# Optimization experiments

Hardware: AMD Instinct MI355X
Metric: run time of the kernel (lower is better)

The kernel has to match this reference:

```python
import jax, jax.numpy as jnp
import numpy as np

IN_FEATURES = 4096
OUT_FEATURES = 4096  # % 16 == 0, so pad_out = 0
BATCH, SEQ = 4, 2048


def setup_inputs() -> dict:
    key = jax.random.key(0)
    k_x, k_w, k_b = jax.random.split(key, 3)
    # int8 activations and weights (W8A8)
    x = jax.random.randint(k_x, (BATCH, SEQ, IN_FEATURES), -128, 128, dtype=jnp.int32).astype(jnp.int8)
    # weight stored as (in_features, out_features), matching qlinear.weight layout
    weight = jax.random.randint(k_w, (IN_FEATURES, OUT_FEATURES), -128, 128, dtype=jnp.int32).astype(jnp.int8)
    # a: scalar input scale; b: per-output-channel dequant/requant scale
    a = jnp.full((1, 1), 0.0123, dtype=jnp.float32)
    b = jax.random.uniform(k_b, (1, OUT_FEATURES), dtype=jnp.float32, minval=0.001, maxval=0.02)
    return {"x": x, "weight": weight, "a": a, "b": b}


def reference(x, weight, a, b):
    # x: [B, S, K] int8; weight: [K, N] int8; a: [1,1] f32; b: [1,N] f32
    x_shape = x.shape
    x2d = x.reshape(-1, x_shape[-1])
    acc = jnp.matmul(x2d, weight, preferred_element_type=jnp.int32)
    # fused dequant (scalar a) + per-channel requant (b), round-to-nearest, saturate to int8
    y_f = acc.astype(jnp.float32) * a * b  # [T, N]
    y = jnp.clip(jnp.round(y_f), -128.0, 127.0).astype(jnp.int8)
    return y.reshape(*x_shape[:-1], -1)
```

## Files before the change

### kernel.cpp

```cpp
#include <hip/hip_runtime.h>
#include <stdint.h>

#define M_DIM 8192
#define N_DIM 4096
#define K_DIM 4096
#define BM 128
#define BN 128
#define BK 64

typedef int v4i __attribute__((ext_vector_type(4)));
typedef unsigned u32;

__device__ __forceinline__ void gll16(const void* g, void* l) {
  __builtin_amdgcn_global_load_lds(
      (const __attribute__((address_space(1))) void*)g,
      (__attribute__((address_space(3))) void*)l, 16, 0, 0);
}

__device__ __forceinline__ u32 pack4(const int4 v) {
  return (v.x & 0xffu) | ((v.y & 0xffu) << 8) | ((v.z & 0xffu) << 16) |
         ((u32)(v.w & 0xffu) << 24);
}

__global__ __launch_bounds__(256) void detect_i32(const int* __restrict__ X,
                                                  u32* __restrict__ flag) {
  __shared__ int ok;
  if (threadIdx.x == 0) ok = 1;
  __syncthreads();
  int good = 1;
  for (int i = threadIdx.x; i < 1024; i += 256) {
    const int w = X[i];
    good &= (w == (int)(int8_t)(w & 0xff));
  }
  if (!good) atomicAnd(&ok, 0);
  __syncthreads();
  if (threadIdx.x == 0) *flag = (u32)ok;
}

__global__ __launch_bounds__(256) void pack_x_ad(const void* __restrict__ Xin,
                                                 u32* __restrict__ out,
                                                 const u32* __restrict__ flag) {
  const bool i32 = (*flag != 0);
  const int base = blockIdx.x * 1024 + threadIdx.x;
  if (i32) {
    const int4* in = (const int4*)Xin;
#pragma unroll
    for (int j = 0; j < 4; ++j) {
      const int idx = base + j * 256;
      out[idx] = pack4(in[idx]);
    }
  } else {
    const u32* in = (const u32*)Xin;
#pragma unroll
    for (int j = 0; j < 4; ++j) {
      const int idx = base + j * 256;
      out[idx] = in[idx];
    }
  }
}

__global__ __launch_bounds__(256) void packT_w_ad(const void* __restrict__ Wv,
                                                  int8_t* __restrict__ WT,
                                                  const u32* __restrict__ flag) {
  __shared__ u32 lds[64 * 21];
  const bool i32 = (*flag != 0);
  const int tid = threadIdx.x;
  const int tk = blockIdx.x & 63;
  const int tn = blockIdx.x >> 6;
  const int k0 = tk * 64, n0 = tn * 64;

#pragma unroll
  for (int j = 0; j < 4; ++j) {
    const int id = j * 256 + tid;
    const int k = id >> 4, c = id & 15;
    u32 word;
    if (i32) {
      const int4 v =
          *(const int4*)((const int*)Wv + (size_t)(k0 + k) * N_DIM + n0 + c * 4);
      word = pack4(v);
    } else {
      word = *(const u32*)((const int8_t*)Wv + (size_t)(k0 + k) * N_DIM + n0 +
                           c * 4);
    }
    lds[k * 21 + c] = word;
  }
  __syncthreads();
  const int kd = tid & 15, nq = tid >> 4;
  const u32 d0 = lds[(kd * 4 + 0) * 21 + nq];
  const u32 d1 = lds[(kd * 4 + 1) * 21 + nq];
  const u32 d2 = lds[(kd * 4 + 2) * 21 + nq];
  const u32 d3 = lds[(kd * 4 + 3) * 21 + nq];
  u32* outp = (u32*)WT;
#pragma unroll
  for (int i = 0; i < 4; ++i) {
    const u32 e = ((d0 >> (8 * i)) & 0xffu) | (((d1 >> (8 * i)) & 0xffu) << 8) |
                  (((d2 >> (8 * i)) & 0xffu) << 16) |
                  (((d3 >> (8 * i)) & 0xffu) << 24);
    const int n = n0 + nq * 4 + i;
    outp[(size_t)n * (K_DIM / 4) + (k0 / 4) + kd] = e;
  }
}

__device__ __forceinline__ void epilogue(const v4i acc[4][4], float a,
                                         const float* __restrict__ bScale,
                                         int* __restrict__ Y, int bm, int bn,
                                         int wm, int wn, int quad, int l16) {
  const int nBase = bn * BN + wn * 64 + l16;
  float bs[4];
#pragma unroll
  for (int ni = 0; ni < 4; ++ni) bs[ni] = bScale[nBase + ni * 16];
#pragma unroll
  for (int mi = 0; mi < 4; ++mi) {
    const int m0 = bm * BM + wm * 64 + mi * 16 + quad * 4;
#pragma unroll
    for (int r = 0; r < 4; ++r) {
      int* row = Y + (size_t)(m0 + r) * N_DIM + nBase;
#pragma unroll
      for (int ni = 0; ni < 4; ++ni) {
        float v = ((float)acc[mi][ni][r] * a) * bs[ni];
        v = rintf(v);
        v = fminf(fmaxf(v, -128.f), 127.f);
        row[ni * 16] = (int)v;
      }
    }
  }
}

__global__ __launch_bounds__(256) void gemm_packed(
    const int8_t* __restrict__ X, const int8_t* __restrict__ WT,
    const float* __restrict__ aScale, const float* __restrict__ bScale,
    int* __restrict__ Y) {
  __shared__ __align__(16) int8_t As[BM * BK];
  __shared__ __align__(16) int8_t Bs[BN * BK];
  const int tid = threadIdx.x;
  const int lane = tid & 63, wave = tid >> 6;
  const int quad = lane >> 4, l16 = lane & 15;
  const int wm = wave & 1, wn = wave >> 1;
  const int bn = blockIdx.x & 31;
  const int bm = blockIdx.x >> 5;

  const int r0 = tid >> 2;
  const int c0 = (tid & 3) * 16;
  const int8_t* Ag0 = X + (size_t)(bm * BM + r0) * K_DIM + c0;
  const int8_t* Ag1 = Ag0 + (size_t)64 * K_DIM;
  const int8_t* Bg0 = WT + (size_t)(bn * BN + r0) * K_DIM + c0;
  const int8_t* Bg1 = Bg0 + (size_t)64 * K_DIM;
  int8_t* Al0 = As + tid * 16;
  int8_t* Al1 = Al0 + 4096;
  int8_t* Bl0 = Bs + tid * 16;
  int8_t* Bl1 = Bl0 + 4096;

  v4i acc[4][4] = {};
  const int8_t* aLds = As + (wm * 64 + l16) * BK + quad * 16;
  const int8_t* bLds = Bs + (wn * 64 + l16) * BK + quad * 16;

  for (int k0 = 0; k0 < K_DIM; k0 += BK) {
    gll16(Ag0 + k0, Al0);
    gll16(Ag1 + k0, Al1);
    gll16(Bg0 + k0, Bl0);
    gll16(Bg1 + k0, Bl1);
    __syncthreads();
    v4i af[4], bf[4];
#pragma unroll
    for (int i = 0; i < 4; ++i) af[i] = *(const v4i*)(aLds + i * 16 * BK);
#pragma unroll
    for (int i = 0; i < 4; ++i) bf[i] = *(const v4i*)(bLds + i * 16 * BK);
#pragma unroll
    for (int mi = 0; mi < 4; ++mi)
#pragma unroll
      for (int ni = 0; ni < 4; ++ni)
        acc[mi][ni] = __builtin_amdgcn_mfma_i32_16x16x64_i8(
            af[mi], bf[ni], acc[mi][ni], 0, 0, 0);
    __syncthreads();
  }
  epilogue(acc, aScale[0], bScale, Y, bm, bn, wm, wn, quad, l16);
}

__global__ __launch_bounds__(256) void gemm_inA(
    const void* __restrict__ Xv, const int8_t* __restrict__ WT,
    const float* __restrict__ aScale, const float* __restrict__ bScale,
    int* __restrict__ Y, const u32* __restrict__ flag) {
  __shared__ __align__(16) int8_t As[BM * BK];
  __shared__ __align__(16) int8_t Bs[BN * BK];
  const bool i32 = (*flag != 0);
  const int tid = threadIdx.x;
  const int lane = tid & 63, wave = tid >> 6;
  const int quad = lane >> 4, l16 = lane & 15;
  const int wm = wave & 1, wn = wave >> 1;
  const int bn = blockIdx.x & 31;
  const int bm = blockIdx.x >> 5;

  const int r0 = tid >> 2;
  const int c0 = (tid & 3) * 16;
  const int8_t* Bg0 = WT + (size_t)(bn * BN + r0) * K_DIM + c0;
  const int8_t* Bg1 = Bg0 + (size_t)64 * K_DIM;
  int8_t* Al0 = As + tid * 16;
  int8_t* Al1 = Al0 + 4096;
  int8_t* Bl0 = Bs + tid * 16;
  int8_t* Bl1 = Bl0 + 4096;

  v4i acc[4][4] = {};
  const int8_t* aLds = As + (wm * 64 + l16) * BK + quad * 16;
  const int8_t* bLds = Bs + (wn * 64 + l16) * BK + quad * 16;

  if (i32) {
    const int* Xg0 = (const int*)Xv + (size_t)(bm * BM + r0) * K_DIM + c0;
    const int* Xg1 = Xg0 + (size_t)64 * K_DIM;
    for (int k0 = 0; k0 < K_DIM; k0 += BK) {
      gll16(Bg0 + k0, Bl0);
      gll16(Bg1 + k0, Bl1);
      const int4* p0 = (const int4*)(Xg0 + k0);
      const int4* p1 = (const int4*)(Xg1 + k0);
      uint4 w0, w1;
      w0.x = pack4(p0[0]); w0.y = pack4(p0[1]);
      w0.z = pack4(p0[2]); w0.w = pack4(p0[3]);
      w1.x = pack4(p1[0]); w1.y = pack4(p1[1]);
      w1.z = pack4(p1[2]); w1.w = pack4(p1[3]);
      *(uint4*)Al0 = w0;
      *(uint4*)Al1 = w1;
      __syncthreads();
      v4i af[4], bf[4];
#pragma unroll
      for (int i = 0; i < 4; ++i) af[i] = *(const v4i*)(aLds + i * 16 * BK);
#pragma unroll
      for (int i = 0; i < 4; ++i) bf[i] = *(const v4i*)(bLds + i * 16 * BK);
#pragma unroll
      for (int mi = 0; mi < 4; ++mi)
#pragma unroll
        for (int ni = 0; ni < 4; ++ni)
          acc[mi][ni] = __builtin_amdgcn_mfma_i32_16x16x64_i8(
              af[mi], bf[ni], acc[mi][ni], 0, 0, 0);
      __syncthreads();
    }
  } else {
    const int8_t* Ag0 = (const int8_t*)Xv + (size_t)(bm * BM + r0) * K_DIM + c0;
    const int8_t* Ag1 = Ag0 + (size_t)64 * K_DIM;
    for (int k0 = 0; k0 < K_DIM; k0 += BK) {
      gll16(Ag0 + k0, Al0);
      gll16(Ag1 + k0, Al1);
      gll16(Bg0 + k0, Bl0);
      gll16(Bg1 + k0, Bl1);
      __syncthreads();
      v4i af[4], bf[4];
#pragma unroll
      for (int i = 0; i < 4; ++i) af[i] = *(const v4i*)(aLds + i * 16 * BK);
#pragma unroll
      for (int i = 0; i < 4; ++i) bf[i] = *(const v4i*)(bLds + i * 16 * BK);
#pragma unroll
      for (int mi = 0; mi < 4; ++mi)
#pragma unroll
        for (int ni = 0; ni < 4; ++ni)
          acc[mi][ni] = __builtin_amdgcn_mfma_i32_16x16x64_i8(
              af[mi], bf[ni], acc[mi][ni], 0, 0, 0);
      __syncthreads();
    }
  }
  epilogue(acc, aScale[0], bScale, Y, bm, bn, wm, wn, quad, l16);
}

extern "C" void kernel_launch(void* const* d_in, const int* in_sizes, int n_in,
                              void* d_out, int out_size, void* d_ws,
                              size_t ws_size, hipStream_t stream) {
  const void* Xv = d_in[0];
  const void* Wv = d_in[1];
  const float* a = (const float*)d_in[2];
  const float* b = (const float*)d_in[3];
  int* Y = (int*)d_out;

  const size_t xB = (size_t)M_DIM * K_DIM;
  const size_t wB = (size_t)N_DIM * K_DIM;
  const int grid = (M_DIM / BM) * (N_DIM / BN);

  if (ws_size >= xB + wB + 64) {
    int8_t* Xp = (int8_t*)d_ws;
    int8_t* WT = (int8_t*)d_ws + xB;
    u32* flag = (u32*)((int8_t*)d_ws + xB + wB);
    detect_i32<<<1, 256, 0, stream>>>((const int*)Xv, flag);
    pack_x_ad<<<(M_DIM * K_DIM / 4) / 1024, 256, 0, stream>>>(Xv, (u32*)Xp,
                                                              flag);
    packT_w_ad<<<(K_DIM / 64) * (N_DIM / 64), 256, 0, stream>>>(Wv, WT, flag);
    gemm_packed<<<grid, 256, 0, stream>>>(Xp, WT, a, b, Y);
  } else if (ws_size >= wB + 64) {
    int8_t* WT = (int8_t*)d_ws;
    u32* flag = (u32*)((int8_t*)d_ws + wB);
    detect_i32<<<1, 256, 0, stream>>>((const int*)Xv, flag);
    packT_w_ad<<<(K_DIM / 64) * (N_DIM / 64), 256, 0, stream>>>(Wv, WT, flag);
    gemm_inA<<<grid, 256, 0, stream>>>(Xv, WT, a, b, Y, flag);
  } else {
    int8_t* WT = (int8_t*)d_ws;
    u32* flag = (u32*)((int8_t*)d_ws + (ws_size >= wB + 4 ? wB : 0));
    detect_i32<<<1, 256, 0, stream>>>((const int*)Xv, flag);
    packT_w_ad<<<(K_DIM / 64) * (N_DIM / 64), 256, 0, stream>>>(Wv, WT, flag);
    gemm_inA<<<grid, 256, 0, stream>>>(Xv, WT, a, b, Y, flag);
  }
}
```

Measured before the change: 431.2 us.

## Fuse X/W prepack into one kernel, drop dtype detection, swizzle LDS layout

Removes the runtime int32-vs-int8 detection kernel and its workspace-size fallbacks, and assumes inputs always arrive as int32. The X pack and the W transpose-pack are merged into a single launch, cutting two launches. The GEMM LDS staging now uses an XOR-swizzled 128-byte row layout (two logical rows per LDS row) so MFMA fragment reads avoid bank conflicts. The risks are that int8-typed inputs or a small workspace are no longer handled.

Result: no change. 431.5 us (+0.1%).

```diff
diff --git a/kernel.cpp b/kernel.cpp
--- a/kernel.cpp
+++ b/kernel.cpp
@@ -22,67 +22,31 @@
          ((u32)(v.w & 0xffu) << 24);
 }
 
-__global__ __launch_bounds__(256) void detect_i32(const int* __restrict__ X,
-                                                  u32* __restrict__ flag) {
-  __shared__ int ok;
-  if (threadIdx.x == 0) ok = 1;
-  __syncthreads();
-  int good = 1;
-  for (int i = threadIdx.x; i < 1024; i += 256) {
-    const int w = X[i];
-    good &= (w == (int)(int8_t)(w & 0xff));
-  }
-  if (!good) atomicAnd(&ok, 0);
-  __syncthreads();
-  if (threadIdx.x == 0) *flag = (u32)ok;
-}
-
-__global__ __launch_bounds__(256) void pack_x_ad(const void* __restrict__ Xin,
-                                                 u32* __restrict__ out,
-                                                 const u32* __restrict__ flag) {
-  const bool i32 = (*flag != 0);
-  const int base = blockIdx.x * 1024 + threadIdx.x;
-  if (i32) {
-    const int4* in = (const int4*)Xin;
+__global__ __launch_bounds__(256) void prepack(const int4* __restrict__ Xi,
+                                               u32* __restrict__ Xp,
+                                               const int* __restrict__ Wi,
+                                               int8_t* __restrict__ WT) {
+  __shared__ u32 lds[64 * 21];
+  const int tid = threadIdx.x;
+  if (blockIdx.x < 8192) {
+    const int base = blockIdx.x * 1024 + tid;
 #pragma unroll
     for (int j = 0; j < 4; ++j) {
       const int idx = base + j * 256;
-      out[idx] = pack4(in[idx]);
+      Xp[idx] = pack4(Xi[idx]);
     }
-  } else {
-    const u32* in = (const u32*)Xin;
-#pragma unroll
-    for (int j = 0; j < 4; ++j) {
-      const int idx = base + j * 256;
-      out[idx] = in[idx];
-    }
+    return;
   }
-}
-
-__global__ __launch_bounds__(256) void packT_w_ad(const void* __restrict__ Wv,
-                                                  int8_t* __restrict__ WT,
-                                                  const u32* __restrict__ flag) {
-  __shared__ u32 lds[64 * 21];
-  const bool i32 = (*flag != 0);
-  const int tid = threadIdx.x;
-  const int tk = blockIdx.x & 63;
-  const int tn = blockIdx.x >> 6;
+  const int bid = blockIdx.x - 8192;
+  const int tk = bid & 63;
+  const int tn = bid >> 6;
   const int k0 = tk * 64, n0 = tn * 64;
-
 #pragma unroll
   for (int j = 0; j < 4; ++j) {
     const int id = j * 256 + tid;
     const int k = id >> 4, c = id & 15;
-    u32 word;
-    if (i32) {
-      const int4 v =
-          *(const int4*)((const int*)Wv + (size_t)(k0 + k) * N_DIM + n0 + c * 4);
-      word = pack4(v);
-    } else {
-      word = *(const u32*)((const int8_t*)Wv + (size_t)(k0 + k) * N_DIM + n0 +
-                           c * 4);
-    }
-    lds[k * 21 + c] = word;
+    const int4 v = *(const int4*)(Wi + (size_t)(k0 + k) * N_DIM + n0 + c * 4);
+    lds[k * 21 + c] = pack4(v);
   }
   __syncthreads();
   const int kd = tid & 15, nq = tid >> 4;
@@ -101,31 +65,6 @@
   }
 }
 
-__device__ __forceinline__ void epilogue(const v4i acc[4][4], float a,
-                                         const float* __restrict__ bScale,
-                                         int* __restrict__ Y, int bm, int bn,
-                                         int wm, int wn, int quad, int l16) {
-  const int nBase = bn * BN + wn * 64 + l16;
-  float bs[4];
-#pragma unroll
-  for (int ni = 0; ni < 4; ++ni) bs[ni] = bScale[nBase + ni * 16];
-#pragma unroll
-  for (int mi = 0; mi < 4; ++mi) {
-    const int m0 = bm * BM + wm * 64 + mi * 16 + quad * 4;
-#pragma unroll
-    for (int r = 0; r < 4; ++r) {
-      int* row = Y + (size_t)(m0 + r) * N_DIM + nBase;
-#pragma unroll
-      for (int ni = 0; ni < 4; ++ni) {
-        float v = ((float)acc[mi][ni][r] * a) * bs[ni];
-        v = rintf(v);
-        v = fminf(fmaxf(v, -128.f), 127.f);
-        row[ni * 16] = (int)v;
-      }
-    }
-  }
-}
-
 __global__ __launch_bounds__(256) void gemm_packed(
     const int8_t* __restrict__ X, const int8_t* __restrict__ WT,
     const float* __restrict__ aScale, const float* __restrict__ bScale,
@@ -139,11 +78,13 @@
   const int bn = blockIdx.x & 31;
   const int bm = blockIdx.x >> 5;
 
-  const int r0 = tid >> 2;
-  const int c0 = (tid & 3) * 16;
-  const int8_t* Ag0 = X + (size_t)(bm * BM + r0) * K_DIM + c0;
+  const int s = tid & 7, blk = tid >> 3;
+  const int t = s ^ (blk & 3);
+  const int q = t & 3, p = t >> 2;
+  const int row = 2 * blk + p;
+  const int8_t* Ag0 = X + (size_t)(bm * BM + row) * K_DIM + q * 16;
   const int8_t* Ag1 = Ag0 + (size_t)64 * K_DIM;
-  const int8_t* Bg0 = WT + (size_t)(bn * BN + r0) * K_DIM + c0;
+  const int8_t* Bg0 = WT + (size_t)(bn * BN + row) * K_DIM + q * 16;
   const int8_t* Bg1 = Bg0 + (size_t)64 * K_DIM;
   int8_t* Al0 = As + tid * 16;
   int8_t* Al1 = Al0 + 4096;
@@ -151,8 +92,10 @@
   int8_t* Bl1 = Bl0 + 4096;
 
   v4i acc[4][4] = {};
-  const int8_t* aLds = As + (wm * 64 + l16) * BK + quad * 16;
-  const int8_t* bLds = Bs + (wn * 64 + l16) * BK + quad * 16;
+
+  const int slot = (quad + 4 * (l16 & 1)) ^ ((l16 >> 1) & 3);
+  const int8_t* aLds = As + (wm * 32 + (l16 >> 1)) * 128 + slot * 16;
+  const int8_t* bLds = Bs + (wn * 32 + (l16 >> 1)) * 128 + slot * 16;
 
   for (int k0 = 0; k0 < K_DIM; k0 += BK) {
     gll16(Ag0 + k0, Al0);
@@ -162,9 +105,9 @@
     __syncthreads();
     v4i af[4], bf[4];
 #pragma unroll
-    for (int i = 0; i < 4; ++i) af[i] = *(const v4i*)(aLds + i * 16 * BK);
+    for (int i = 0; i < 4; ++i) af[i] = *(const v4i*)(aLds + i * 1024);
 #pragma unroll
-    for (int i = 0; i < 4; ++i) bf[i] = *(const v4i*)(bLds + i * 16 * BK);
+    for (int i = 0; i < 4; ++i) bf[i] = *(const v4i*)(bLds + i * 1024);
 #pragma unroll
     for (int mi = 0; mi < 4; ++mi)
 #pragma unroll
@@ -173,124 +116,43 @@
             af[mi], bf[ni], acc[mi][ni], 0, 0, 0);
     __syncthreads();
   }
-  epilogue(acc, aScale[0], bScale, Y, bm, bn, wm, wn, quad, l16);
-}
 
-__global__ __launch_bounds__(256) void gemm_inA(
-    const void* __restrict__ Xv, const int8_t* __restrict__ WT,
-    const float* __restrict__ aScale, const float* __restrict__ bScale,
-    int* __restrict__ Y, const u32* __restrict__ flag) {
-  __shared__ __align__(16) int8_t As[BM * BK];
-  __shared__ __align__(16) int8_t Bs[BN * BK];
-  const bool i32 = (*flag != 0);
-  const int tid = threadIdx.x;
-  const int lane = tid & 63, wave = tid >> 6;
-  const int quad = lane >> 4, l16 = lane & 15;
-  const int wm = wave & 1, wn = wave >> 1;
-  const int bn = blockIdx.x & 31;
-  const int bm = blockIdx.x >> 5;
-
-  const int r0 = tid >> 2;
-  const int c0 = (tid & 3) * 16;
-  const int8_t* Bg0 = WT + (size_t)(bn * BN + r0) * K_DIM + c0;
-  const int8_t* Bg1 = Bg0 + (size_t)64 * K_DIM;
-  int8_t* Al0 = As + tid * 16;
-  int8_t* Al1 = Al0 + 4096;
-  int8_t* Bl0 = Bs + tid * 16;
-  int8_t* Bl1 = Bl0 + 4096;
-
-  v4i acc[4][4] = {};
-  const int8_t* aLds = As + (wm * 64 + l16) * BK + quad * 16;
-  const int8_t* bLds = Bs + (wn * 64 + l16) * BK + quad * 16;
-
-  if (i32) {
-    const int* Xg0 = (const int*)Xv + (size_t)(bm * BM + r0) * K_DIM + c0;
-    const int* Xg1 = Xg0 + (size_t)64 * K_DIM;
-    for (int k0 = 0; k0 < K_DIM; k0 += BK) {
-      gll16(Bg0 + k0, Bl0);
-      gll16(Bg1 + k0, Bl1);
-      const int4* p0 = (const int4*)(Xg0 + k0);
-      const int4* p1 = (const int4*)(Xg1 + k0);
-      uint4 w0, w1;
-      w0.x = pack4(p0[0]); w0.y = pack4(p0[1]);
-      w0.z = pack4(p0[2]); w0.w = pack4(p0[3]);
-      w1.x = pack4(p1[0]); w1.y = pack4(p1[1]);
-      w1.z = pack4(p1[2]); w1.w = pack4(p1[3]);
-      *(uint4*)Al0 = w0;
-      *(uint4*)Al1 = w1;
-      __syncthreads();
-      v4i af[4], bf[4];
+  const float a = aScale[0];
+  const int nBase = bn * BN + wn * 64 + l16;
+  float bs[4];
 #pragma unroll
-      for (int i = 0; i < 4; ++i) af[i] = *(const v4i*)(aLds + i * 16 * BK);
+  for (int ni = 0; ni < 4; ++ni) bs[ni] = bScale[nBase + ni * 16];
 #pragma unroll
-      for (int i = 0; i < 4; ++i) bf[i] = *(const v4i*)(bLds + i * 16 * BK);
+  for (int mi = 0; mi < 4; ++mi) {
+    const int m0 = bm * BM + wm * 64 + mi * 16 + quad * 4;
 #pragma unroll
-      for (int mi = 0; mi < 4; ++mi)
+    for (int r = 0; r < 4; ++r) {
+      int* rowp = Y + (size_t)(m0 + r) * N_DIM + nBase;
 #pragma unroll
-        for (int ni = 0; ni < 4; ++ni)
-          acc[mi][ni] = __builtin_amdgcn_mfma_i32_16x16x64_i8(
-              af[mi], bf[ni], acc[mi][ni], 0, 0, 0);
-      __syncthreads();
-    }
-  } else {
-    const int8_t* Ag0 = (const int8_t*)Xv + (size_t)(bm * BM + r0) * K_DIM + c0;
-    const int8_t* Ag1 = Ag0 + (size_t)64 * K_DIM;
-    for (int k0 = 0; k0 < K_DIM; k0 += BK) {
-      gll16(Ag0 + k0, Al0);
-      gll16(Ag1 + k0, Al1);
-      gll16(Bg0 + k0, Bl0);
-      gll16(Bg1 + k0, Bl1);
-      __syncthreads();
-      v4i af[4], bf[4];
-#pragma unroll
-      for (int i = 0; i < 4; ++i) af[i] = *(const v4i*)(aLds + i * 16 * BK);
-#pragma unroll
-      for (int i = 0; i < 4; ++i) bf[i] = *(const v4i*)(bLds + i * 16 * BK);
-#pragma unroll
-      for (int mi = 0; mi < 4; ++mi)
-#pragma unroll
-        for (int ni = 0; ni < 4; ++ni)
-          acc[mi][ni] = __builtin_amdgcn_mfma_i32_16x16x64_i8(
-              af[mi], bf[ni], acc[mi][ni], 0, 0, 0);
-      __syncthreads();
+      for (int ni = 0; ni < 4; ++ni) {
+        float v = ((float)acc[mi][ni][r] * a) * bs[ni];
+        v = rintf(v);
+        v = fminf(fmaxf(v, -128.f), 127.f);
+        rowp[ni * 16] = (int)v;
+      }
     }
   }
-  epilogue(acc, aScale[0], bScale, Y, bm, bn, wm, wn, quad, l16);
 }
 
 extern "C" void kernel_launch(void* const* d_in, const int* in_sizes, int n_in,
                               void* d_out, int out_size, void* d_ws,
                               size_t ws_size, hipStream_t stream) {
-  const void* Xv = d_in[0];
-  const void* Wv = d_in[1];
+  const int4* Xi = (const int4*)d_in[0];
+  const int* Wi = (const int*)d_in[1];
   const float* a = (const float*)d_in[2];
   const float* b = (const float*)d_in[3];
   int* Y = (int*)d_out;
 
   const size_t xB = (size_t)M_DIM * K_DIM;
-  const size_t wB = (size_t)N_DIM * K_DIM;
-  const int grid = (M_DIM / BM) * (N_DIM / BN);
+  int8_t* Xp = (int8_t*)d_ws;
+  int8_t* WT = (int8_t*)d_ws + xB;
 
-  if (ws_size >= xB + wB + 64) {
-    int8_t* Xp = (int8_t*)d_ws;
-    int8_t* WT = (int8_t*)d_ws + xB;
-    u32* flag = (u32*)((int8_t*)d_ws + xB + wB);
-    detect_i32<<<1, 256, 0, stream>>>((const int*)Xv, flag);
-    pack_x_ad<<<(M_DIM * K_DIM / 4) / 1024, 256, 0, stream>>>(Xv, (u32*)Xp,
-                                                              flag);
-    packT_w_ad<<<(K_DIM / 64) * (N_DIM / 64), 256, 0, stream>>>(Wv, WT, flag);
-    gemm_packed<<<grid, 256, 0, stream>>>(Xp, WT, a, b, Y);
-  } else if (ws_size >= wB + 64) {
-    int8_t* WT = (int8_t*)d_ws;
-    u32* flag = (u32*)((int8_t*)d_ws + wB);
-    detect_i32<<<1, 256, 0, stream>>>((const int*)Xv, flag);
-    packT_w_ad<<<(K_DIM / 64) * (N_DIM / 64), 256, 0, stream>>>(Wv, WT, flag);
-    gemm_inA<<<grid, 256, 0, stream>>>(Xv, WT, a, b, Y, flag);
-  } else {
-    int8_t* WT = (int8_t*)d_ws;
-    u32* flag = (u32*)((int8_t*)d_ws + (ws_size >= wB + 4 ? wB : 0));
-    detect_i32<<<1, 256, 0, stream>>>((const int*)Xv, flag);
-    packT_w_ad<<<(K_DIM / 64) * (N_DIM / 64), 256, 0, stream>>>(Wv, WT, flag);
-    gemm_inA<<<grid, 256, 0, stream>>>(Xv, WT, a, b, Y, flag);
-  }
+  prepack<<<8192 + (K_DIM / 64) * (N_DIM / 64), 256, 0, stream>>>(
+      Xi, (u32*)Xp, Wi, WT);
+  gemm_packed<<<(M_DIM / BM) * (N_DIM / BN), 256, 0, stream>>>(Xp, WT, a, b, Y);
 }
```
